# Kernel tuning notes

Measured on AMD Instinct MI355X. Metric: run time of the kernel, lower is better.

The kernel has to match this reference:

```python
import jax, jax.numpy as jnp
import numpy as np

N_NODES = 100000


def gcn_layer(x, src, dst, W, b):
    """PyG GCNConv: add self-loops, symmetric deg normalization, XW then scatter-add."""
    n = x.shape[0]
    loop = jnp.arange(n, dtype=src.dtype)
    s = jnp.concatenate([src, loop])
    d = jnp.concatenate([dst, loop])
    # degree of target nodes (includes self-loop)
    deg = jax.ops.segment_sum(jnp.ones_like(d, dtype=x.dtype), d, num_segments=n)
    dinv = jnp.where(deg > 0, jax.lax.rsqrt(deg), 0.0)
    norm = dinv[s] * dinv[d]                      # [E+N]
    h = x @ W                                     # [N, out]
    msg = h[s] * norm[:, None]                    # [E+N, out]
    out = jax.ops.segment_sum(msg, d, num_segments=n) + b
    return out


def setup_inputs() -> dict:
    key = jax.random.key(0)
    k1, k2, k3, k4 = jax.random.split(key, 4)
    d_in, d_hid, d_out = 256, 256, 128
    E = 3200000
    x = jax.random.normal(k1, (N_NODES, d_in), dtype=jnp.float32)
    edge_index = jax.random.randint(k2, (2, E), 0, N_NODES, dtype=jnp.int64)
    # glorot-style init for GCN weights
    W1 = jax.random.normal(k3, (d_in, d_hid), dtype=jnp.float32) / np.sqrt(d_in)
    b1 = jnp.zeros((d_hid,), dtype=jnp.float32)
    W2 = jax.random.normal(k4, (d_hid, d_out), dtype=jnp.float32) / np.sqrt(d_hid)
    b2 = jnp.zeros((d_out,), dtype=jnp.float32)
    return {"x": x, "W1": W1, "b1": b1, "W2": W2, "b2": b2, "edge_index": edge_index}


def reference(x, W1, b1, W2, b2, edge_index):
    src, dst = edge_index[0], edge_index[1]
    h = jax.nn.relu(gcn_layer(x, src, dst, W1, b1))
    out = jax.nn.relu(gcn_layer(h, src, dst, W2, b2))
    return out
```

## Files before the change

### kernel.cpp

```cpp
#include <hip/hip_runtime.h>


typedef short          s16x8 __attribute__((ext_vector_type(8)));
typedef float          f32x4 __attribute__((ext_vector_type(4)));
typedef unsigned short u16x4 __attribute__((ext_vector_type(4)));
typedef unsigned short u16x2 __attribute__((ext_vector_type(2)));

__device__ __forceinline__ float bf2f(unsigned short u) {
  union { unsigned int i; float f; } x; x.i = ((unsigned int)u) << 16; return x.f;
}
__device__ __forceinline__ unsigned short f2bf(float f) {
  union { float f; unsigned int i; } x; x.f = f;
  unsigned int r = x.i + 0x7FFFu + ((x.i >> 16) & 1u);
  return (unsigned short)(r >> 16);
}


#define NBUCK_PAD 1024
#define BIN_CHUNK 8192

__global__ void k_zero1024(int* __restrict__ p) { p[threadIdx.x + blockIdx.x * 256] = 0; }

__global__ __launch_bounds__(256) void k_hist(const int* __restrict__ dst,
                                              int* __restrict__ bcnt, int E) {
  __shared__ int h[NBUCK_PAD];
  int t = threadIdx.x;
  for (int i = t; i < NBUCK_PAD; i += 256) h[i] = 0;
  __syncthreads();
  int stride = gridDim.x * 256;
  for (int e = blockIdx.x * 256 + t; e < E; e += stride) atomicAdd(&h[dst[e] >> 7], 1);
  __syncthreads();
  for (int i = t; i < NBUCK_PAD; i += 256) {
    int v = h[i];
    if (v) atomicAdd(bcnt + i, v);
  }
}

__global__ void k_bscan(const int* __restrict__ bcnt, int* __restrict__ bptr,
                        int* __restrict__ bcur, int* __restrict__ rowptr, int M, int E) {
  __shared__ int sh[NBUCK_PAD];
  int t = threadIdx.x;
  int v = bcnt[t];
  sh[t] = v; __syncthreads();
  int x = v;
  for (int off = 1; off < NBUCK_PAD; off <<= 1) {
    int y = (t >= off) ? sh[t - off] : 0;
    __syncthreads();
    x += y; sh[t] = x;
    __syncthreads();
  }
  bptr[t] = x - v;
  bcur[t] = x - v;
  if (t == NBUCK_PAD - 1) bptr[NBUCK_PAD] = x;
  if (t == 0) rowptr[M] = E;
}

__global__ __launch_bounds__(256) void k_bin(const int* __restrict__ src,
                                             const int* __restrict__ dst,
                                             int* __restrict__ bcur,
                                             unsigned int* __restrict__ binned, int E) {
  __shared__ int hist[NBUCK_PAD];
  __shared__ int base[NBUCK_PAD];
  int t = threadIdx.x;
  int e0 = blockIdx.x * BIN_CHUNK;
  int e1 = min(e0 + BIN_CHUNK, E);
  for (int i = t; i < NBUCK_PAD; i += 256) hist[i] = 0;
  __syncthreads();
  for (int e = e0 + t; e < e1; e += 256) atomicAdd(&hist[dst[e] >> 7], 1);
  __syncthreads();
  for (int i = t; i < NBUCK_PAD; i += 256) {
    int h = hist[i];
    base[i] = h ? atomicAdd(bcur + i, h) : 0;
    hist[i] = 0;
  }
  __syncthreads();
  for (int e = e0 + t; e < e1; e += 256) {
    int d = dst[e], s = src[e];
    int b = d >> 7;
    int p = base[b] + atomicAdd(&hist[b], 1);
    binned[p] = ((unsigned)(d & 127) << 17) | (unsigned)s;
  }
}

__global__ __launch_bounds__(256) void k_csr(const unsigned int* __restrict__ binned,
                                             const int* __restrict__ bptr,
                                             int* __restrict__ rowptr,
                                             float* __restrict__ dinv,
                                             int* __restrict__ col, int M) {
  __shared__ int deg[128];
  __shared__ int sc[128];
  __shared__ int cur[128];
  int b = blockIdx.x, t = threadIdx.x;
  int n0 = b << 7;
  int nn = min(128, M - n0);
  int e0 = bptr[b], e1 = bptr[b + 1];
  if (t < 128) deg[t] = 0;
  __syncthreads();
  for (int e = e0 + t; e < e1; e += 256) atomicAdd(&deg[(binned[e] >> 17) & 127], 1);
  __syncthreads();
  if (t < 128) sc[t] = deg[t];
  __syncthreads();
  for (int off = 1; off < 128; off <<= 1) {
    int y = 0;
    if (t < 128 && t >= off) y = sc[t - off];
    __syncthreads();
    if (t < 128) sc[t] += y;
    __syncthreads();
  }
  if (t < nn) {
    int excl = sc[t] - deg[t];
    rowptr[n0 + t] = e0 + excl;
    dinv[n0 + t] = rsqrtf((float)(deg[t] + 1));
    cur[t] = excl;
  }
  __syncthreads();
  for (int e = e0 + t; e < e1; e += 256) {
    unsigned v = binned[e];
    int dl = (v >> 17) & 127;
    int p = e0 + atomicAdd(&cur[dl], 1);
    col[p] = (int)(v & 0x1FFFFu);
  }
}


__global__ void k_cvt(const float* __restrict__ x, unsigned short* __restrict__ xb, int n4) {
  int i = blockIdx.x * 256 + threadIdx.x;
  if (i < n4) {
    float4 v = ((const float4*)x)[i];
    u16x4 o; o[0] = f2bf(v.x); o[1] = f2bf(v.y); o[2] = f2bf(v.z); o[3] = f2bf(v.w);
    ((u16x4*)xb)[i] = o;
  }
}

__global__ void k_cvt_wt(const float* __restrict__ W, unsigned short* __restrict__ Wt,
                         int K, int N) {
  int i = blockIdx.x * 256 + threadIdx.x;
  if (i < K * N) {
    int k = i / N, n = i % N;
    Wt[n * K + k] = f2bf(W[i]);
  }
}


__device__ __forceinline__ int swz(int row, int kc) { return kc ^ ((row & 3) << 3); }

__global__ __launch_bounds__(256) void k_gemm(
    const unsigned short* __restrict__ A, const unsigned short* __restrict__ Bt,
    const float* __restrict__ dinv, unsigned short* __restrict__ G, int M, int N) {
  const int K = 256;
  __shared__ short lA[128 * 32];
  __shared__ short lB[64 * 32];
  int tid = threadIdx.x;
  int wid = tid >> 6, lane = tid & 63;
  int l15 = lane & 15;
  int lkg = (lane >> 4) * 8;
  int bm = blockIdx.x * 128;
  int bn = blockIdx.y * 64;

  f32x4 acc[2][4] = {};

  for (int kt = 0; kt < 8; ++kt) {
    int k0 = kt * 32;
    __syncthreads();
#pragma unroll
    for (int h = 0; h < 2; ++h) {
      int cid = tid + h * 256;
      int r = cid >> 2, kc = (cid & 3) * 8;
      int gr = bm + r;
      s16x8 v = {0, 0, 0, 0, 0, 0, 0, 0};
      if (gr < M) v = *(const s16x8*)(A + (size_t)gr * K + k0 + kc);
      *(s16x8*)(&lA[r * 32 + swz(r, kc)]) = v;
    }
    {
      int c = tid >> 2, kc = (tid & 3) * 8;
      s16x8 v = *(const s16x8*)(Bt + (size_t)(bn + c) * K + k0 + kc);
      *(s16x8*)(&lB[c * 32 + swz(c, kc)]) = v;
    }
    __syncthreads();

    s16x8 af[2], bfr[4];
#pragma unroll
    for (int mi = 0; mi < 2; ++mi) {
      int r = wid * 32 + mi * 16 + l15;
      af[mi] = *(const s16x8*)(&lA[r * 32 + swz(r, lkg)]);
    }
#pragma unroll
    for (int ni = 0; ni < 4; ++ni) {
      int c = ni * 16 + l15;
      bfr[ni] = *(const s16x8*)(&lB[c * 32 + swz(c, lkg)]);
    }
#pragma unroll
    for (int mi = 0; mi < 2; ++mi)
#pragma unroll
      for (int ni = 0; ni < 4; ++ni)
        acc[mi][ni] = __builtin_amdgcn_mfma_f32_16x16x32_bf16(af[mi], bfr[ni], acc[mi][ni], 0, 0, 0);
  }

#pragma unroll
  for (int mi = 0; mi < 2; ++mi) {
    int mrow0 = bm + wid * 32 + mi * 16 + (lane >> 4) * 4;
#pragma unroll
    for (int j = 0; j < 4; ++j) {
      int m = mrow0 + j;
      if (m < M) {
        float dv = dinv[m];
#pragma unroll
        for (int ni = 0; ni < 4; ++ni) {
          float val = acc[mi][ni][j] * dv;
          G[(size_t)m * N + bn + ni * 16 + l15] = f2bf(val);
        }
      }
    }
  }
}


__global__ __launch_bounds__(256) void k_agg256(
    const unsigned short* __restrict__ G, const int* __restrict__ rowptr,
    const int* __restrict__ col, const float* __restrict__ dinv,
    const float* __restrict__ bias, unsigned short* __restrict__ H, int M) {
  int lane = threadIdx.x & 63;
  int v = (blockIdx.x << 2) + (threadIdx.x >> 6);
  if (v >= M) return;
  int c4 = lane * 4;
  size_t base = (size_t)v * 256 + c4;
  float a0, a1, a2, a3;
  {
    u16x4 s = *(const u16x4*)(G + base);
    a0 = bf2f(s[0]); a1 = bf2f(s[1]); a2 = bf2f(s[2]); a3 = bf2f(s[3]);
  }
  int jb = rowptr[v], je = rowptr[v + 1];
  int j = jb;
  for (; j + 3 < je; j += 4) {
    int u0 = col[j], u1 = col[j + 1], u2 = col[j + 2], u3 = col[j + 3];
    u16x4 p0 = *(const u16x4*)(G + (size_t)u0 * 256 + c4);
    u16x4 p1 = *(const u16x4*)(G + (size_t)u1 * 256 + c4);
    u16x4 p2 = *(const u16x4*)(G + (size_t)u2 * 256 + c4);
    u16x4 p3 = *(const u16x4*)(G + (size_t)u3 * 256 + c4);
    a0 += bf2f(p0[0]) + bf2f(p1[0]) + bf2f(p2[0]) + bf2f(p3[0]);
    a1 += bf2f(p0[1]) + bf2f(p1[1]) + bf2f(p2[1]) + bf2f(p3[1]);
    a2 += bf2f(p0[2]) + bf2f(p1[2]) + bf2f(p2[2]) + bf2f(p3[2]);
    a3 += bf2f(p0[3]) + bf2f(p1[3]) + bf2f(p2[3]) + bf2f(p3[3]);
  }
  for (; j < je; ++j) {
    int u = col[j];
    u16x4 p = *(const u16x4*)(G + (size_t)u * 256 + c4);
    a0 += bf2f(p[0]); a1 += bf2f(p[1]); a2 += bf2f(p[2]); a3 += bf2f(p[3]);
  }
  float dv = dinv[v];
  float4 bb = *(const float4*)(bias + c4);
  u16x4 o;
  o[0] = f2bf(fmaxf(fmaf(dv, a0, bb.x), 0.f));
  o[1] = f2bf(fmaxf(fmaf(dv, a1, bb.y), 0.f));
  o[2] = f2bf(fmaxf(fmaf(dv, a2, bb.z), 0.f));
  o[3] = f2bf(fmaxf(fmaf(dv, a3, bb.w), 0.f));
  *(u16x4*)(H + base) = o;
}

__global__ __launch_bounds__(256) void k_agg128(
    const unsigned short* __restrict__ G, const int* __restrict__ rowptr,
    const int* __restrict__ col, const float* __restrict__ dinv,
    const float* __restrict__ bias, float* __restrict__ Out, int M) {
  int lane = threadIdx.x & 63;
  int v = (blockIdx.x << 2) + (threadIdx.x >> 6);
  if (v >= M) return;
  int c2 = lane * 2;
  size_t base = (size_t)v * 128 + c2;
  float a0, a1;
  {
    u16x2 s = *(const u16x2*)(G + base);
    a0 = bf2f(s[0]); a1 = bf2f(s[1]);
  }
  int jb = rowptr[v], je = rowptr[v + 1];
  int j = jb;
  for (; j + 3 < je; j += 4) {
    int u0 = col[j], u1 = col[j + 1], u2 = col[j + 2], u3 = col[j + 3];
    u16x2 p0 = *(const u16x2*)(G + (size_t)u0 * 128 + c2);
    u16x2 p1 = *(const u16x2*)(G + (size_t)u1 * 128 + c2);
    u16x2 p2 = *(const u16x2*)(G + (size_t)u2 * 128 + c2);
    u16x2 p3 = *(const u16x2*)(G + (size_t)u3 * 128 + c2);
    a0 += bf2f(p0[0]) + bf2f(p1[0]) + bf2f(p2[0]) + bf2f(p3[0]);
    a1 += bf2f(p0[1]) + bf2f(p1[1]) + bf2f(p2[1]) + bf2f(p3[1]);
  }
  for (; j < je; ++j) {
    int u = col[j];
    u16x2 p = *(const u16x2*)(G + (size_t)u * 128 + c2);
    a0 += bf2f(p[0]); a1 += bf2f(p[1]);
  }
  float dv = dinv[v];
  float2 r;
  r.x = fmaxf(fmaf(dv, a0, bias[c2 + 0]), 0.f);
  r.y = fmaxf(fmaf(dv, a1, bias[c2 + 1]), 0.f);
  *(float2*)(Out + base) = r;
}


extern "C" void kernel_launch(void* const* d_in, const int* in_sizes, int n_in,
                              void* d_out, int out_size, void* d_ws, size_t ws_size,
                              hipStream_t stream) {
  const float* x  = (const float*)d_in[0];
  const float* W1 = (const float*)d_in[1];
  const float* b1 = (const float*)d_in[2];
  const float* W2 = (const float*)d_in[3];
  const float* b2 = (const float*)d_in[4];
  const int*   ei = (const int*)d_in[5];

  const int D_IN = 256, D_HID = 256, D_OUT = 128;
  const int M = in_sizes[0] / D_IN;
  const int E = in_sizes[5] / 2;
  const int* src = ei;
  const int* dst = ei + E;

  char* p = (char*)d_ws;
  auto alloc = [&](size_t bytes) { void* r = (void*)p; p += (bytes + 255) & ~(size_t)255; return r; };
  float* dinv = (float*)alloc((size_t)M * 4);
  int* rowptr = (int*)alloc((size_t)(M + 1) * 4);
  int* bcnt   = (int*)alloc(NBUCK_PAD * 4);
  int* bptr   = (int*)alloc((NBUCK_PAD + 1) * 4);
  int* bcur   = (int*)alloc(NBUCK_PAD * 4);
  int* colx   = (int*)alloc((size_t)E * 4);
  unsigned short* xb  = (unsigned short*)alloc((size_t)M * D_IN * 2);
  unsigned short* w1t = (unsigned short*)alloc((size_t)D_HID * D_IN * 2);
  unsigned short* w2t = (unsigned short*)alloc((size_t)D_OUT * D_HID * 2);
  unsigned short* g1  = (unsigned short*)alloc((size_t)M * D_HID * 2);
  unsigned short* hid = (unsigned short*)alloc((size_t)M * D_HID * 2);
  unsigned short* g2  = xb;
  unsigned int* binned = (unsigned int*)hid;

  int nbuck = (M + 127) >> 7;
  int nbin  = (E + BIN_CHUNK - 1) / BIN_CHUNK;

  k_zero1024<<<4, 256, 0, stream>>>(bcnt);
  k_hist <<<256, 256, 0, stream>>>(dst, bcnt, E);
  k_bscan<<<1, NBUCK_PAD, 0, stream>>>(bcnt, bptr, bcur, rowptr, M, E);
  k_bin  <<<nbin, 256, 0, stream>>>(src, dst, bcur, binned, E);
  k_csr  <<<nbuck, 256, 0, stream>>>(binned, bptr, rowptr, dinv, colx, M);

  k_cvt   <<<(M * D_IN / 4 + 255) / 256, 256, 0, stream>>>(x, xb, M * D_IN / 4);
  k_cvt_wt<<<(D_IN * D_HID + 255) / 256, 256, 0, stream>>>(W1, w1t, D_IN, D_HID);
  k_cvt_wt<<<(D_HID * D_OUT + 255) / 256, 256, 0, stream>>>(W2, w2t, D_HID, D_OUT);

  dim3 gg1((M + 127) / 128, D_HID / 64);
  k_gemm  <<<gg1, 256, 0, stream>>>(xb, w1t, dinv, g1, M, D_HID);
  k_agg256<<<(M + 3) / 4, 256, 0, stream>>>(g1, rowptr, colx, dinv, b1, hid, M);

  dim3 gg2((M + 127) / 128, D_OUT / 64);
  k_gemm  <<<gg2, 256, 0, stream>>>(hid, w2t, dinv, g2, M, D_OUT);
  k_agg128<<<(M + 3) / 4, 256, 0, stream>>>(g2, rowptr, colx, dinv, b2, (float*)d_out, M);
}
```

Baseline: 577.3 us.

## Fuse x conversion into GEMM1 and fuse layer-1 aggregation with GEMM2

After: 779.6 us. +35.0%, slower.

```diff
diff --git a/kernel.cpp b/kernel.cpp
--- a/kernel.cpp
+++ b/kernel.cpp
@@ -123,15 +123,6 @@
 }
 
 
-__global__ void k_cvt(const float* __restrict__ x, unsigned short* __restrict__ xb, int n4) {
-  int i = blockIdx.x * 256 + threadIdx.x;
-  if (i < n4) {
-    float4 v = ((const float4*)x)[i];
-    u16x4 o; o[0] = f2bf(v.x); o[1] = f2bf(v.y); o[2] = f2bf(v.z); o[3] = f2bf(v.w);
-    ((u16x4*)xb)[i] = o;
-  }
-}
-
 __global__ void k_cvt_wt(const float* __restrict__ W, unsigned short* __restrict__ Wt,
                          int K, int N) {
   int i = blockIdx.x * 256 + threadIdx.x;
@@ -142,63 +133,66 @@
 }
 
 
-__device__ __forceinline__ int swz(int row, int kc) { return kc ^ ((row & 3) << 3); }
-
-__global__ __launch_bounds__(256) void k_gemm(
-    const unsigned short* __restrict__ A, const unsigned short* __restrict__ Bt,
-    const float* __restrict__ dinv, unsigned short* __restrict__ G, int M, int N) {
+__device__ __forceinline__ int swz4(int row, int kc) { return kc ^ ((row & 3) << 3); }
+
+__global__ __launch_bounds__(512) void k_gemm1(
+    const float* __restrict__ X, const unsigned short* __restrict__ Bt,
+    const float* __restrict__ dinv, unsigned short* __restrict__ G, int M) {
   const int K = 256;
   __shared__ short lA[128 * 32];
-  __shared__ short lB[64 * 32];
+  __shared__ short lB[256 * 32];
   int tid = threadIdx.x;
   int wid = tid >> 6, lane = tid & 63;
+  int wm = wid >> 2, wn = wid & 3;
   int l15 = lane & 15;
   int lkg = (lane >> 4) * 8;
   int bm = blockIdx.x * 128;
-  int bn = blockIdx.y * 64;
-
-  f32x4 acc[2][4] = {};
+
+  f32x4 acc[4][4] = {};
 
   for (int kt = 0; kt < 8; ++kt) {
     int k0 = kt * 32;
     __syncthreads();
 #pragma unroll
     for (int h = 0; h < 2; ++h) {
-      int cid = tid + h * 256;
-      int r = cid >> 2, kc = (cid & 3) * 8;
+      int cid = tid + h * 512;
+      int r = cid >> 3, c4 = (cid & 7) * 4;
       int gr = bm + r;
-      s16x8 v = {0, 0, 0, 0, 0, 0, 0, 0};
-      if (gr < M) v = *(const s16x8*)(A + (size_t)gr * K + k0 + kc);
-      *(s16x8*)(&lA[r * 32 + swz(r, kc)]) = v;
-    }
-    {
-      int c = tid >> 2, kc = (tid & 3) * 8;
-      s16x8 v = *(const s16x8*)(Bt + (size_t)(bn + c) * K + k0 + kc);
-      *(s16x8*)(&lB[c * 32 + swz(c, kc)]) = v;
-    }
-    __syncthreads();
-
-    s16x8 af[2], bfr[4];
-#pragma unroll
-    for (int mi = 0; mi < 2; ++mi) {
-      int r = wid * 32 + mi * 16 + l15;
-      af[mi] = *(const s16x8*)(&lA[r * 32 + swz(r, lkg)]);
+      float4 v = {0.f, 0.f, 0.f, 0.f};
+      if (gr < M) v = *(const float4*)(X + (size_t)gr * K + k0 + c4);
+      u16x4 o; o[0] = f2bf(v.x); o[1] = f2bf(v.y); o[2] = f2bf(v.z); o[3] = f2bf(v.w);
+      *(u16x4*)(&lA[r * 32 + swz4(r, c4)]) = o;
+    }
+#pragma unroll
+    for (int h = 0; h < 2; ++h) {
+      int cid = tid + h * 512;
+      int n = cid >> 2, kc = (cid & 3) * 8;
+      s16x8 v = *(const s16x8*)(Bt + (size_t)n * K + k0 + kc);
+      *(s16x8*)(&lB[n * 32 + swz4(n, kc)]) = v;
+    }
+    __syncthreads();
+
+    s16x8 af[4], bfr[4];
+#pragma unroll
+    for (int mi = 0; mi < 4; ++mi) {
+      int r = wm * 64 + mi * 16 + l15;
+      af[mi] = *(const s16x8*)(&lA[r * 32 + swz4(r, lkg)]);
     }
 #pragma unroll
     for (int ni = 0; ni < 4; ++ni) {
-      int c = ni * 16 + l15;
-      bfr[ni] = *(const s16x8*)(&lB[c * 32 + swz(c, lkg)]);
-    }
-#pragma unroll
-    for (int mi = 0; mi < 2; ++mi)
+      int c = wn * 64 + ni * 16 + l15;
+      bfr[ni] = *(const s16x8*)(&lB[c * 32 + swz4(c, lkg)]);
+    }
+#pragma unroll
+    for (int mi = 0; mi < 4; ++mi)
 #pragma unroll
       for (int ni = 0; ni < 4; ++ni)
         acc[mi][ni] = __builtin_amdgcn_mfma_f32_16x16x32_bf16(af[mi], bfr[ni], acc[mi][ni], 0, 0, 0);
   }
 
 #pragma unroll
-  for (int mi = 0; mi < 2; ++mi) {
-    int mrow0 = bm + wid * 32 + mi * 16 + (lane >> 4) * 4;
+  for (int mi = 0; mi < 4; ++mi) {
+    int mrow0 = bm + wm * 64 + mi * 16 + (lane >> 4) * 4;
 #pragma unroll
     for (int j = 0; j < 4; ++j) {
       int m = mrow0 + j;
@@ -206,8 +200,7 @@
         float dv = dinv[m];
 #pragma unroll
         for (int ni = 0; ni < 4; ++ni) {
-          float val = acc[mi][ni][j] * dv;
-          G[(size_t)m * N + bn + ni * 16 + l15] = f2bf(val);
+          G[(size_t)m * 256 + wn * 64 + ni * 16 + l15] = f2bf(acc[mi][ni][j] * dv);
         }
       }
     }
@@ -215,47 +208,93 @@
 }
 
 
-__global__ __launch_bounds__(256) void k_agg256(
+__global__ __launch_bounds__(256) void k_agg_gemm(
     const unsigned short* __restrict__ G, const int* __restrict__ rowptr,
     const int* __restrict__ col, const float* __restrict__ dinv,
-    const float* __restrict__ bias, unsigned short* __restrict__ H, int M) {
-  int lane = threadIdx.x & 63;
-  int v = (blockIdx.x << 2) + (threadIdx.x >> 6);
-  if (v >= M) return;
+    const float* __restrict__ bias, const unsigned short* __restrict__ W2t,
+    unsigned short* __restrict__ G2, int M) {
+  __shared__ short lH[128 * 256];
+  int tid = threadIdx.x;
+  int w = tid >> 6, lane = tid & 63;
+  int l15 = lane & 15;
+  int lkg = (lane >> 4) * 8;
+  int n0 = blockIdx.x << 7;
   int c4 = lane * 4;
-  size_t base = (size_t)v * 256 + c4;
-  float a0, a1, a2, a3;
-  {
-    u16x4 s = *(const u16x4*)(G + base);
-    a0 = bf2f(s[0]); a1 = bf2f(s[1]); a2 = bf2f(s[2]); a3 = bf2f(s[3]);
-  }
-  int jb = rowptr[v], je = rowptr[v + 1];
-  int j = jb;
-  for (; j + 3 < je; j += 4) {
-    int u0 = col[j], u1 = col[j + 1], u2 = col[j + 2], u3 = col[j + 3];
-    u16x4 p0 = *(const u16x4*)(G + (size_t)u0 * 256 + c4);
-    u16x4 p1 = *(const u16x4*)(G + (size_t)u1 * 256 + c4);
-    u16x4 p2 = *(const u16x4*)(G + (size_t)u2 * 256 + c4);
-    u16x4 p3 = *(const u16x4*)(G + (size_t)u3 * 256 + c4);
-    a0 += bf2f(p0[0]) + bf2f(p1[0]) + bf2f(p2[0]) + bf2f(p3[0]);
-    a1 += bf2f(p0[1]) + bf2f(p1[1]) + bf2f(p2[1]) + bf2f(p3[1]);
-    a2 += bf2f(p0[2]) + bf2f(p1[2]) + bf2f(p2[2]) + bf2f(p3[2]);
-    a3 += bf2f(p0[3]) + bf2f(p1[3]) + bf2f(p2[3]) + bf2f(p3[3]);
-  }
-  for (; j < je; ++j) {
-    int u = col[j];
-    u16x4 p = *(const u16x4*)(G + (size_t)u * 256 + c4);
-    a0 += bf2f(p[0]); a1 += bf2f(p[1]); a2 += bf2f(p[2]); a3 += bf2f(p[3]);
-  }
-  float dv = dinv[v];
   float4 bb = *(const float4*)(bias + c4);
-  u16x4 o;
-  o[0] = f2bf(fmaxf(fmaf(dv, a0, bb.x), 0.f));
-  o[1] = f2bf(fmaxf(fmaf(dv, a1, bb.y), 0.f));
-  o[2] = f2bf(fmaxf(fmaf(dv, a2, bb.z), 0.f));
-  o[3] = f2bf(fmaxf(fmaf(dv, a3, bb.w), 0.f));
-  *(u16x4*)(H + base) = o;
-}
+
+  for (int i = 0; i < 32; ++i) {
+    int vl = w * 32 + i;
+    int v = n0 + vl;
+    float a0 = 0.f, a1 = 0.f, a2 = 0.f, a3 = 0.f;
+    if (v < M) {
+      size_t base = (size_t)v * 256 + c4;
+      u16x4 s = *(const u16x4*)(G + base);
+      a0 = bf2f(s[0]); a1 = bf2f(s[1]); a2 = bf2f(s[2]); a3 = bf2f(s[3]);
+      int jb = rowptr[v], je = rowptr[v + 1];
+      int j = jb;
+      for (; j + 3 < je; j += 4) {
+        int u0 = col[j], u1 = col[j + 1], u2 = col[j + 2], u3 = col[j + 3];
+        u16x4 p0 = *(const u16x4*)(G + (size_t)u0 * 256 + c4);
+        u16x4 p1 = *(const u16x4*)(G + (size_t)u1 * 256 + c4);
+        u16x4 p2 = *(const u16x4*)(G + (size_t)u2 * 256 + c4);
+        u16x4 p3 = *(const u16x4*)(G + (size_t)u3 * 256 + c4);
+        a0 += bf2f(p0[0]) + bf2f(p1[0]) + bf2f(p2[0]) + bf2f(p3[0]);
+        a1 += bf2f(p0[1]) + bf2f(p1[1]) + bf2f(p2[1]) + bf2f(p3[1]);
+        a2 += bf2f(p0[2]) + bf2f(p1[2]) + bf2f(p2[2]) + bf2f(p3[2]);
+        a3 += bf2f(p0[3]) + bf2f(p1[3]) + bf2f(p2[3]) + bf2f(p3[3]);
+      }
+      for (; j < je; ++j) {
+        int u = col[j];
+        u16x4 p = *(const u16x4*)(G + (size_t)u * 256 + c4);
+        a0 += bf2f(p[0]); a1 += bf2f(p[1]); a2 += bf2f(p[2]); a3 += bf2f(p[3]);
+      }
+      float dv = dinv[v];
+      a0 = fmaxf(fmaf(dv, a0, bb.x), 0.f);
+      a1 = fmaxf(fmaf(dv, a1, bb.y), 0.f);
+      a2 = fmaxf(fmaf(dv, a2, bb.z), 0.f);
+      a3 = fmaxf(fmaf(dv, a3, bb.w), 0.f);
+    }
+    u16x4 o; o[0] = f2bf(a0); o[1] = f2bf(a1); o[2] = f2bf(a2); o[3] = f2bf(a3);
+    *(u16x4*)(&lH[vl * 256 + (c4 ^ ((vl & 7) << 3))]) = o;
+  }
+  __syncthreads();
+
+  f32x4 acc[8][2] = {};
+#pragma unroll
+  for (int kt = 0; kt < 8; ++kt) {
+    int k0 = kt * 32;
+    s16x8 bfr[2];
+#pragma unroll
+    for (int nf = 0; nf < 2; ++nf) {
+      int n = w * 32 + nf * 16 + l15;
+      bfr[nf] = *(const s16x8*)(W2t + (size_t)n * 256 + k0 + lkg);
+    }
+#pragma unroll
+    for (int mf = 0; mf < 8; ++mf) {
+      int row = mf * 16 + l15;
+      s16x8 af = *(const s16x8*)(&lH[row * 256 + ((k0 + lkg) ^ ((row & 7) << 3))]);
+#pragma unroll
+      for (int nf = 0; nf < 2; ++nf)
+        acc[mf][nf] = __builtin_amdgcn_mfma_f32_16x16x32_bf16(af, bfr[nf], acc[mf][nf], 0, 0, 0);
+    }
+  }
+
+#pragma unroll
+  for (int mf = 0; mf < 8; ++mf) {
+    int ml0 = mf * 16 + (lane >> 4) * 4;
+#pragma unroll
+    for (int j = 0; j < 4; ++j) {
+      int node = n0 + ml0 + j;
+      if (node < M) {
+        float dv = dinv[node];
+#pragma unroll
+        for (int nf = 0; nf < 2; ++nf)
+          G2[(size_t)node * 128 + w * 32 + nf * 16 + l15] = f2bf(acc[mf][nf][j] * dv);
+      }
+    }
+  }
+}
+
 
 __global__ __launch_bounds__(256) void k_agg128(
     const unsigned short* __restrict__ G, const int* __restrict__ rowptr,
@@ -319,13 +358,11 @@
   int* bptr   = (int*)alloc((NBUCK_PAD + 1) * 4);
   int* bcur   = (int*)alloc(NBUCK_PAD * 4);
   int* colx   = (int*)alloc((size_t)E * 4);
-  unsigned short* xb  = (unsigned short*)alloc((size_t)M * D_IN * 2);
   unsigned short* w1t = (unsigned short*)alloc((size_t)D_HID * D_IN * 2);
   unsigned short* w2t = (unsigned short*)alloc((size_t)D_OUT * D_HID * 2);
   unsigned short* g1  = (unsigned short*)alloc((size_t)M * D_HID * 2);
-  unsigned short* hid = (unsigned short*)alloc((size_t)M * D_HID * 2);
-  unsigned short* g2  = xb;
-  unsigned int* binned = (unsigned int*)hid;
+  unsigned short* g2  = (unsigned short*)alloc((size_t)M * D_OUT * 2);
+  unsigned int* binned = (unsigned int*)g1;
 
   int nbuck = (M + 127) >> 7;
   int nbin  = (E + BIN_CHUNK - 1) / BIN_CHUNK;
@@ -336,15 +373,10 @@
   k_bin  <<<nbin, 256, 0, stream>>>(src, dst, bcur, binned, E);
   k_csr  <<<nbuck, 256, 0, stream>>>(binned, bptr, rowptr, dinv, colx, M);
 
-  k_cvt   <<<(M * D_IN / 4 + 255) / 256, 256, 0, stream>>>(x, xb, M * D_IN / 4);
   k_cvt_wt<<<(D_IN * D_HID + 255) / 256, 256, 0, stream>>>(W1, w1t, D_IN, D_HID);
   k_cvt_wt<<<(D_HID * D_OUT + 255) / 256, 256, 0, stream>>>(W2, w2t, D_HID, D_OUT);
 
-  dim3 gg1((M + 127) / 128, D_HID / 64);
-  k_gemm  <<<gg1, 256, 0, stream>>>(xb, w1t, dinv, g1, M, D_HID);
-  k_agg256<<<(M + 3) / 4, 256, 0, stream>>>(g1, rowptr, colx, dinv, b1, hid, M);
-
-  dim3 gg2((M + 127) / 128, D_OUT / 64);
-  k_gemm  <<<gg2, 256, 0, stream>>>(hid, w2t, dinv, g2, M, D_OUT);
-  k_agg128<<<(M + 3) / 4, 256, 0, stream>>>(g2, rowptr, colx, dinv, b2, (float*)d_out, M);
-}
+  k_gemm1   <<<nbuck, 512, 0, stream>>>(x, w1t, dinv, g1, M);
+  k_agg_gemm<<<nbuck, 256, 0, stream>>>(g1, rowptr, colx, dinv, b1, w2t, g2, M);
+  k_agg128  <<<(M + 3) / 4, 256, 0, stream>>>(g2, rowptr, colx, dinv, b2, (float*)d_out, M);
+}
```
